# Performance work log

Measured on AMD Instinct MI355X. Metric: run time of the kernel, lower is better.

## Reference

```python
import jax, jax.numpy as jnp
import numpy as np

NUM_GRAPHS = 64

def setup_inputs() -> dict:
    key = jax.random.key(0)
    ks = jax.random.split(key, 10)
    N, E, D, V = 100000, 1600000, 64, 30
    node_types = jax.random.randint(ks[0], (N,), 0, V, dtype=jnp.int64 if jax.config.jax_enable_x64 else jnp.int32)
    edge_index = jax.random.randint(ks[1], (2, E), 0, N, dtype=jnp.int32)
    batch = jnp.sort(jax.random.randint(ks[2], (N,), 0, NUM_GRAPHS, dtype=jnp.int32))
    emb_table = jax.random.normal(ks[3], (V, D), dtype=jnp.float32)
    W1 = jax.random.normal(ks[4], (D, D), dtype=jnp.float32) / np.sqrt(D)
    W2 = jax.random.normal(ks[5], (D, D), dtype=jnp.float32) / np.sqrt(D)
    W3 = jax.random.normal(ks[6], (D, D), dtype=jnp.float32) / np.sqrt(D)
    b1 = jnp.zeros((D,), jnp.float32)
    b2 = jnp.zeros((D,), jnp.float32)
    b3 = jnp.zeros((D,), jnp.float32)
    return {"node_types": node_types, "edge_index": edge_index, "batch": batch,
            "emb_table": emb_table, "W1": W1, "b1": b1, "W2": W2, "b2": b2, "W3": W3, "b3": b3}

def _gcn_conv(x, W, b, row, col, norm, N):
    # x' = D^-1/2 (A+I) D^-1/2 (x @ W) + b   (PyG GCNConv semantics)
    h = x @ W
    msg = h[row] * norm[:, None]              # gather + edgewise scale
    out = jax.ops.segment_sum(msg, col, num_segments=N)  # scatter-add at targets
    return out + b

def reference(node_types, edge_index, batch, emb_table, W1, b1, W2, b2, W3, b3):
    N = node_types.shape[0]
    # add self-loops
    loops = jnp.arange(N, dtype=edge_index.dtype)
    row = jnp.concatenate([edge_index[0], loops])
    col = jnp.concatenate([edge_index[1], loops])
    # symmetric normalization on A + I
    deg = jax.ops.segment_sum(jnp.ones_like(col, dtype=jnp.float32), col, num_segments=N)
    dinv = jnp.where(deg > 0, jax.lax.rsqrt(deg), 0.0)
    norm = dinv[row] * dinv[col]
    x = emb_table[node_types]
    x = jax.nn.relu(_gcn_conv(x, W1, b1, row, col, norm, N))
    x = jax.nn.relu(_gcn_conv(x, W2, b2, row, col, norm, N))
    x = _gcn_conv(x, W3, b3, row, col, norm, N)
    # global mean pool over batch segments
    sums = jax.ops.segment_sum(x, batch, num_segments=NUM_GRAPHS)
    cnts = jax.ops.segment_sum(jnp.ones((N,), jnp.float32), batch, num_segments=NUM_GRAPHS)
    pooled = sums / jnp.maximum(cnts, 1.0)[:, None]
    # L2 normalize rows
    return pooled / jnp.linalg.norm(pooled, axis=1, keepdims=True)
```

## Files before the change

kernel.cpp:

```cpp
#include <hip/hip_runtime.h>
#include <hip/hip_fp16.h>

#define DD 64
#define NUM_GRAPHS 64
#define AGG_BLOCKS 2048
#define EB 512
#define BINW 256
#define MAXNB 512
#define EBIN_CAP 6144

__global__ __launch_bounds__(256) void k_hist(const int* __restrict__ col,
                                              int* __restrict__ H, int E, int NB, int CE) {
    __shared__ int h[MAXNB];
    int eb = blockIdx.x, t = threadIdx.x;
    for (int i = t; i < NB; i += 256) h[i] = 0;
    __syncthreads();
    int e0 = eb * CE, e1 = min(E, e0 + CE);
    for (int e = e0 + t; e < e1; e += 256) atomicAdd(&h[col[e] >> 8], 1);
    __syncthreads();
    for (int i = t; i < NB; i += 256) H[eb * NB + i] = h[i];
}

__global__ __launch_bounds__(256) void k_scanA(int* __restrict__ H,
                                               int* __restrict__ bintot, int NB) {
    __shared__ int s[256];
    int b = blockIdx.x, t = threadIdx.x;
    int i0 = (2 * t) * NB + b, i1 = (2 * t + 1) * NB + b;
    int v0 = H[i0], v1 = H[i1];
    int tot = v0 + v1;
    s[t] = tot;
    __syncthreads();
    for (int off = 1; off < 256; off <<= 1) {
        int tv = (t >= off) ? s[t - off] : 0;
        __syncthreads();
        s[t] += tv;
        __syncthreads();
    }
    int excl = s[t] - tot;
    H[i0] = excl;
    H[i1] = excl + v0;
    if (t == 255) bintot[b] = s[255];
}

__global__ void k_scanB(const int* __restrict__ bintot, int* __restrict__ binstart, int NB) {
    __shared__ int s[512];
    int t = threadIdx.x;
    int v = (t < NB) ? bintot[t] : 0;
    s[t] = v;
    __syncthreads();
    for (int off = 1; off < 512; off <<= 1) {
        int tv = (t >= off) ? s[t - off] : 0;
        __syncthreads();
        s[t] += tv;
        __syncthreads();
    }
    if (t < NB) binstart[t] = s[t] - v;
    if (t == 511) binstart[NB] = s[511];
}

__global__ __launch_bounds__(256) void k_scatbin(const int* __restrict__ row,
                                                 const int* __restrict__ col,
                                                 const int* __restrict__ H,
                                                 const int* __restrict__ binstart,
                                                 unsigned* __restrict__ binned,
                                                 int E, int NB, int CE) {
    __shared__ int off[MAXNB];
    int eb = blockIdx.x, t = threadIdx.x;
    for (int i = t; i < NB; i += 256) off[i] = binstart[i] + H[eb * NB + i];
    __syncthreads();
    int e0 = eb * CE, e1 = min(E, e0 + CE);
    for (int e = e0 + t; e < e1; e += 256) {
        int c = col[e], r = row[e];
        int slot = atomicAdd(&off[c >> 8], 1);
        binned[slot] = ((unsigned)(c & 255) << 24) | (unsigned)r;
    }
}

__global__ __launch_bounds__(256) void k_bincsr(const unsigned* __restrict__ binned,
                                                const int* __restrict__ binstart,
                                                const int* __restrict__ nt,
                                                int* __restrict__ srcidx,
                                                int* __restrict__ rowptr,
                                                float* __restrict__ dinv,
                                                int2* __restrict__ pk, int N, int NB) {
    __shared__ unsigned arr[EBIN_CAP];
    __shared__ int sorted_[EBIN_CAP];
    __shared__ int cnt[BINW];
    __shared__ int base[BINW];
    __shared__ int cursor[BINW];
    int b = blockIdx.x, t = threadIdx.x;
    int s0 = binstart[b], s1 = binstart[b + 1];
    int binsz = s1 - s0;
    if (binsz > EBIN_CAP) binsz = EBIN_CAP;
    cnt[t] = 0;
    for (int i = t; i < binsz; i += 256) arr[i] = binned[s0 + i];
    __syncthreads();
    for (int i = t; i < binsz; i += 256) atomicAdd(&cnt[arr[i] >> 24], 1);
    __syncthreads();
    int v = cnt[t];
    base[t] = v;
    __syncthreads();
    for (int off = 1; off < 256; off <<= 1) {
        int tv = (t >= off) ? base[t - off] : 0;
        __syncthreads();
        base[t] += tv;
        __syncthreads();
    }
    int excl = base[t] - v;
    __syncthreads();
    base[t] = excl;
    cursor[t] = excl;
    __syncthreads();
    for (int i = t; i < binsz; i += 256) {
        unsigned val = arr[i];
        int pos = atomicAdd(&cursor[val >> 24], 1);
        sorted_[pos] = (int)(val & 0xFFFFFF);
    }
    __syncthreads();
    for (int i = t; i < binsz; i += 256) srcidx[s0 + i] = sorted_[i];
    int node = b * BINW + t;
    if (node < N) {
        rowptr[node] = s0 + base[t];
        float di = rsqrtf((float)cnt[t] + 1.0f);
        dinv[node] = di;
        pk[node] = make_int2(nt[node], __float_as_int(di));
    }
    if (b == NB - 1 && t == 0) rowptr[N] = s1;
}

__global__ void k_buildepk(const int* __restrict__ srcidx, const int2* __restrict__ pk,
                           unsigned* __restrict__ epku, int E) {
    int i = blockIdx.x * blockDim.x + threadIdx.x;
    if (i >= E) return;
    int2 p = pk[srcidx[i]];
    epku[i] = ((unsigned)p.x << 16) |
              (unsigned)__half_as_ushort(__float2half(__int_as_float(p.y)));
}

__global__ void k_embW1(const float* __restrict__ emb, const float* __restrict__ W1,
                        float* __restrict__ embW1, int V) {
    __shared__ float er[DD];
    int v = blockIdx.x, j = threadIdx.x;
    er[j] = emb[v * DD + j];
    __syncthreads();
    float acc = 0.0f;
    #pragma unroll
    for (int d = 0; d < DD; ++d) acc += er[d] * W1[d * DD + j];
    embW1[v * DD + j] = acc;
}

__device__ __forceinline__ float rowmatmul(float v, const float* Wcol) {
    int vb = __float_as_int(v);
    float o0 = 0.f, o1 = 0.f, o2 = 0.f, o3 = 0.f;
    #pragma unroll
    for (int d = 0; d < DD; d += 4) {
        o0 = fmaf(__int_as_float(__builtin_amdgcn_readlane(vb, d + 0)), Wcol[d + 0], o0);
        o1 = fmaf(__int_as_float(__builtin_amdgcn_readlane(vb, d + 1)), Wcol[d + 1], o1);
        o2 = fmaf(__int_as_float(__builtin_amdgcn_readlane(vb, d + 2)), Wcol[d + 2], o2);
        o3 = fmaf(__int_as_float(__builtin_amdgcn_readlane(vb, d + 3)), Wcol[d + 3], o3);
    }
    return (o0 + o1) + (o2 + o3);
}

__device__ __forceinline__ float rowmatmul_q(float4 v, const float* Wcol) {
    float va[4] = {v.x, v.y, v.z, v.w};
    int vb[4] = {__float_as_int(v.x), __float_as_int(v.y),
                 __float_as_int(v.z), __float_as_int(v.w)};
    (void)va;
    float o0 = 0.f, o1 = 0.f, o2 = 0.f, o3 = 0.f;
    #pragma unroll
    for (int d = 0; d < DD; d += 4) {
        o0 = fmaf(__int_as_float(__builtin_amdgcn_readlane(vb[0], d >> 2)), Wcol[d + 0], o0);
        o1 = fmaf(__int_as_float(__builtin_amdgcn_readlane(vb[1], d >> 2)), Wcol[d + 1], o1);
        o2 = fmaf(__int_as_float(__builtin_amdgcn_readlane(vb[2], d >> 2)), Wcol[d + 2], o2);
        o3 = fmaf(__int_as_float(__builtin_amdgcn_readlane(vb[3], d >> 2)), Wcol[d + 3], o3);
    }
    return (o0 + o1) + (o2 + o3);
}

__device__ __forceinline__ void acc_h4(float4& a, uint2 r) {
    float2 f0 = __half22float2(*(const __half2*)&r.x);
    float2 f1 = __half22float2(*(const __half2*)&r.y);
    a.x += f0.x; a.y += f0.y; a.z += f1.x; a.w += f1.y;
}

__device__ __forceinline__ float4 gather_sum_q(const int* __restrict__ srcidx,
                                               const __half* __restrict__ Hs,
                                               int s, int e, int g, int l) {
    float4 A = {0,0,0,0}, B = {0,0,0,0}, C = {0,0,0,0}, D = {0,0,0,0};
    int k = s;
    for (; k + 16 <= e; k += 16) {
        int i0 = srcidx[k + g];
        int i1 = srcidx[k + 4 + g];
        int i2 = srcidx[k + 8 + g];
        int i3 = srcidx[k + 12 + g];
        uint2 r0 = *(const uint2*)(Hs + (long)i0 * DD + 4 * l);
        uint2 r1 = *(const uint2*)(Hs + (long)i1 * DD + 4 * l);
        uint2 r2 = *(const uint2*)(Hs + (long)i2 * DD + 4 * l);
        uint2 r3 = *(const uint2*)(Hs + (long)i3 * DD + 4 * l);
        acc_h4(A, r0); acc_h4(B, r1); acc_h4(C, r2); acc_h4(D, r3);
    }
    for (; k < e; k += 4) {
        if (k + g < e) {
            int i0 = srcidx[k + g];
            uint2 r0 = *(const uint2*)(Hs + (long)i0 * DD + 4 * l);
            acc_h4(A, r0);
        }
    }
    A.x += B.x + C.x + D.x; A.y += B.y + C.y + D.y;
    A.z += B.z + C.z + D.z; A.w += B.w + C.w + D.w;
    A.x += __shfl_xor(A.x, 16, 64); A.x += __shfl_xor(A.x, 32, 64);
    A.y += __shfl_xor(A.y, 16, 64); A.y += __shfl_xor(A.y, 32, 64);
    A.z += __shfl_xor(A.z, 16, 64); A.z += __shfl_xor(A.z, 32, 64);
    A.w += __shfl_xor(A.w, 16, 64); A.w += __shfl_xor(A.w, 32, 64);
    return A;
}

__global__ __launch_bounds__(256) void k_agg1_fused(const int* __restrict__ rowptr,
                                                    const unsigned* __restrict__ epku,
                                                    const int2* __restrict__ pk,
                                                    const float* __restrict__ embW1,
                                                    const float* __restrict__ b1,
                                                    const float* __restrict__ W2,
                                                    __half* __restrict__ OUT, int N, int V) {
    __shared__ float ew[30 * DD];
    int tid = threadIdx.x;
    for (int k = tid; k < V * DD; k += 256) ew[k] = embW1[k];
    __syncthreads();
    int j = tid & 63;
    float Wcol[DD];
    #pragma unroll
    for (int d = 0; d < DD; ++d) Wcol[d] = W2[d * DD + j];
    float bj = b1[j];
    int wave0 = blockIdx.x * 4 + (tid >> 6);
    int wstride = gridDim.x * 4;
    for (int node = __builtin_amdgcn_readfirstlane(wave0); node < N;
         node += wstride) {
        int s = rowptr[node], e = rowptr[node + 1];
        float acc = 0.0f;
        int k = s;
        for (; k + 7 < e; k += 8) {
            unsigned u0 = epku[k],   u1 = epku[k+1], u2 = epku[k+2], u3 = epku[k+3];
            unsigned u4 = epku[k+4], u5 = epku[k+5], u6 = epku[k+6], u7 = epku[k+7];
            acc += ew[(u0 >> 16) * DD + j] * __half2float(__ushort_as_half((unsigned short)(u0 & 0xFFFF)))
                 + ew[(u1 >> 16) * DD + j] * __half2float(__ushort_as_half((unsigned short)(u1 & 0xFFFF)))
                 + ew[(u2 >> 16) * DD + j] * __half2float(__ushort_as_half((unsigned short)(u2 & 0xFFFF)))
                 + ew[(u3 >> 16) * DD + j] * __half2float(__ushort_as_half((unsigned short)(u3 & 0xFFFF)));
            acc += ew[(u4 >> 16) * DD + j] * __half2float(__ushort_as_half((unsigned short)(u4 & 0xFFFF)))
                 + ew[(u5 >> 16) * DD + j] * __half2float(__ushort_as_half((unsigned short)(u5 & 0xFFFF)))
                 + ew[(u6 >> 16) * DD + j] * __half2float(__ushort_as_half((unsigned short)(u6 & 0xFFFF)))
                 + ew[(u7 >> 16) * DD + j] * __half2float(__ushort_as_half((unsigned short)(u7 & 0xFFFF)));
        }
        for (; k < e; ++k) {
            unsigned u0 = epku[k];
            acc += ew[(u0 >> 16) * DD + j] * __half2float(__ushort_as_half((unsigned short)(u0 & 0xFFFF)));
        }
        int2 pc = pk[node];
        float dc = __int_as_float(pc.y);
        float v = (acc + ew[pc.x * DD + j] * dc) * dc + bj;
        v = fmaxf(v, 0.0f);
        OUT[(long)node * DD + j] = __float2half(rowmatmul(v, Wcol) * dc);
    }
}

__global__ __launch_bounds__(256) void k_agg2_fused(const int* __restrict__ rowptr,
                                                    const int* __restrict__ srcidx,
                                                    const float* __restrict__ dinv,
                                                    const __half* __restrict__ Hs,
                                                    const float* __restrict__ b2,
                                                    const float* __restrict__ W3,
                                                    __half* __restrict__ OUT, int N) {
    int tid = threadIdx.x;
    int lane = tid & 63;
    int g = lane >> 4, l = lane & 15;
    float Wcol[DD];
    #pragma unroll
    for (int d = 0; d < DD; ++d) Wcol[d] = W3[d * DD + lane];
    float4 bq = *(const float4*)(b2 + 4 * l);
    int wave0 = blockIdx.x * 4 + (tid >> 6);
    int wstride = gridDim.x * 4;
    for (int node = __builtin_amdgcn_readfirstlane(wave0); node < N;
         node += wstride) {
        int s = rowptr[node], e = rowptr[node + 1];
        float4 acc = gather_sum_q(srcidx, Hs, s, e, g, l);
        float dc = dinv[node];
        uint2 sr = *(const uint2*)(Hs + (long)node * DD + 4 * l);
        float2 s0 = __half22float2(*(const __half2*)&sr.x);
        float2 s1 = __half22float2(*(const __half2*)&sr.y);
        float4 v;
        v.x = fmaxf((acc.x + s0.x) * dc + bq.x, 0.f);
        v.y = fmaxf((acc.y + s0.y) * dc + bq.y, 0.f);
        v.z = fmaxf((acc.z + s1.x) * dc + bq.z, 0.f);
        v.w = fmaxf((acc.w + s1.y) * dc + bq.w, 0.f);
        float o = rowmatmul_q(v, Wcol);
        OUT[(long)node * DD + lane] = __float2half(o * dc);
    }
}

__global__ __launch_bounds__(256) void k_agg3_pool(const int* __restrict__ rowptr,
                                                   const int* __restrict__ srcidx,
                                                   const float* __restrict__ dinv,
                                                   const __half* __restrict__ Hs,
                                                   const float* __restrict__ b3,
                                                   const int* __restrict__ batch,
                                                   float* __restrict__ pool,
                                                   int N, int chunk) {
    int tid = threadIdx.x;
    int lane = tid & 63;
    int g = lane >> 4, l = lane & 15;
    int w = __builtin_amdgcn_readfirstlane(blockIdx.x * 4 + (tid >> 6));
    int start = w * chunk;
    if (start >= N) return;
    int endn = min(N, start + chunk);
    float4 bq = *(const float4*)(b3 + 4 * l);
    int gcur = batch[start];
    float4 pacc = {0.f, 0.f, 0.f, 0.f};
    for (int node = start; node < endn; ++node) {
        int s = rowptr[node], e = rowptr[node + 1];
        float4 acc = gather_sum_q(srcidx, Hs, s, e, g, l);
        float dc = dinv[node];
        uint2 sr = *(const uint2*)(Hs + (long)node * DD + 4 * l);
        float2 s0 = __half22float2(*(const __half2*)&sr.x);
        float2 s1 = __half22float2(*(const __half2*)&sr.y);
        float4 v;
        v.x = (acc.x + s0.x) * dc + bq.x;
        v.y = (acc.y + s0.y) * dc + bq.y;
        v.z = (acc.z + s1.x) * dc + bq.z;
        v.w = (acc.w + s1.y) * dc + bq.w;
        int gb = batch[node];
        if (gb != gcur) {
            if (g == 0) {
                atomicAdd(&pool[gcur * DD + 4 * l + 0], pacc.x);
                atomicAdd(&pool[gcur * DD + 4 * l + 1], pacc.y);
                atomicAdd(&pool[gcur * DD + 4 * l + 2], pacc.z);
                atomicAdd(&pool[gcur * DD + 4 * l + 3], pacc.w);
            }
            gcur = gb;
            pacc = v;
        } else {
            pacc.x += v.x; pacc.y += v.y; pacc.z += v.z; pacc.w += v.w;
        }
    }
    if (g == 0) {
        atomicAdd(&pool[gcur * DD + 4 * l + 0], pacc.x);
        atomicAdd(&pool[gcur * DD + 4 * l + 1], pacc.y);
        atomicAdd(&pool[gcur * DD + 4 * l + 2], pacc.z);
        atomicAdd(&pool[gcur * DD + 4 * l + 3], pacc.w);
    }
}

__global__ void k_final(const float* __restrict__ pool, const int* __restrict__ batch,
                        float* __restrict__ out, int N) {
    int g = blockIdx.x, j = threadIdx.x;
    int lo = 0, hi = N;
    while (lo < hi) { int m = (lo + hi) >> 1; if (batch[m] < g) lo = m + 1; else hi = m; }
    int lo2 = lo; hi = N;
    while (lo2 < hi) { int m = (lo2 + hi) >> 1; if (batch[m] < g + 1) lo2 = m + 1; else hi = m; }
    float cnt = fmaxf((float)(lo2 - lo), 1.0f);
    float v = pool[g * DD + j] / cnt;
    float sq = v * v;
    #pragma unroll
    for (int off = 32; off > 0; off >>= 1) sq += __shfl_down(sq, off, 64);
    float nrm = __shfl(sq, 0, 64);
    out[g * DD + j] = v / sqrtf(nrm);
}

extern "C" void kernel_launch(void* const* d_in, const int* in_sizes, int n_in,
                              void* d_out, int out_size, void* d_ws, size_t ws_size,
                              hipStream_t stream) {
    const int*   node_types = (const int*)d_in[0];
    const int*   edge_index = (const int*)d_in[1];
    const int*   batch      = (const int*)d_in[2];
    const float* emb        = (const float*)d_in[3];
    const float* W1 = (const float*)d_in[4];
    const float* b1 = (const float*)d_in[5];
    const float* W2 = (const float*)d_in[6];
    const float* b2 = (const float*)d_in[7];
    const float* W3 = (const float*)d_in[8];
    const float* b3 = (const float*)d_in[9];
    const int N = in_sizes[0];
    const int E = in_sizes[1] / 2;
    const int V = in_sizes[3] / DD;
    const int* row = edge_index;
    const int* col = edge_index + E;
    const long ND = (long)N * DD;
    const int NB = (N + BINW - 1) / BINW;
    const int CE = (E + EB - 1) / EB;

    char* p = (char*)d_ws;
    __half*   hsA     = (__half*)p;       p += ND * sizeof(__half);
    __half*   hsB     = (__half*)p;       p += ND * sizeof(__half);
    int*      srcidx  = (int*)p;          p += (size_t)E * sizeof(int);
    unsigned* epku    = (unsigned*)p;     p += (size_t)E * sizeof(unsigned);
    unsigned* binned  = (unsigned*)p;     p += (size_t)E * sizeof(unsigned);
    int*      H       = (int*)p;          p += (size_t)EB * NB * sizeof(int);
    int*      bintot  = (int*)p;          p += (size_t)(NB + 4) * sizeof(int);
    int*      binstart= (int*)p;          p += (size_t)(NB + 4) * sizeof(int);
    float*    dinv    = (float*)p;        p += (size_t)N * sizeof(float);
    int2*     pk      = (int2*)p;         p += (size_t)N * sizeof(int2);
    int*      rowptr  = (int*)p;          p += (size_t)(N + 4) * sizeof(int);
    float*    pool    = (float*)p;        p += (size_t)NUM_GRAPHS * DD * sizeof(float);
    float*    embW1   = (float*)p;        p += (size_t)V * DD * sizeof(float);

    k_hist<<<EB, 256, 0, stream>>>(col, H, E, NB, CE);
    k_scanA<<<NB, 256, 0, stream>>>(H, bintot, NB);
    k_scanB<<<1, 512, 0, stream>>>(bintot, binstart, NB);
    k_scatbin<<<EB, 256, 0, stream>>>(row, col, H, binstart, binned, E, NB, CE);
    k_bincsr<<<NB, 256, 0, stream>>>(binned, binstart, node_types, srcidx, rowptr,
                                     dinv, pk, N, NB);
    k_buildepk<<<(E + 255) / 256, 256, 0, stream>>>(srcidx, pk, epku, E);

    k_embW1<<<V, DD, 0, stream>>>(emb, W1, embW1, V);
    k_agg1_fused<<<AGG_BLOCKS, 256, 0, stream>>>(rowptr, epku, pk, embW1, b1, W2,
                                                 hsA, N, V);
    k_agg2_fused<<<AGG_BLOCKS, 256, 0, stream>>>(rowptr, srcidx, dinv, hsA, b2, W3,
                                                 hsB, N);
    hipMemsetAsync(pool, 0, (size_t)(NUM_GRAPHS * DD) * sizeof(float), stream);
    const int totalWaves = AGG_BLOCKS * 4;
    const int chunk = (N + totalWaves - 1) / totalWaves;
    k_agg3_pool<<<AGG_BLOCKS, 256, 0, stream>>>(rowptr, srcidx, dinv, hsB, b3, batch,
                                                pool, N, chunk);
    k_final<<<NUM_GRAPHS, DD, 0, stream>>>(pool, batch, (float*)d_out, N);
}
```

Baseline: 318.0 us.

## Use packed fp16 dot2 for fused epilogue matmuls and prefetch gather rows

The W2 and W3 weight columns are pre-packed into half2 pairs by a small new kernel. The per-node 64x64 epilogue matmuls in the layer-1 and layer-2 aggregation kernels now use v_dot2 fp16 instructions with fp32 accumulate, which halves the readlane and FMA count and the per-lane weight registers. Separately, the fp16 neighbor gather loop is software-pipelined so the next 16 rows load before the current ones are accumulated. In exchange, activations and weights in the epilogue are rounded to fp16, which lowers accuracy, and the prefetch raises register pressure.

```diff
diff --git a/kernel.cpp b/kernel.cpp
--- a/kernel.cpp
+++ b/kernel.cpp
@@ -8,6 +8,13 @@
 #define BINW 256
 #define MAXNB 512
 #define EBIN_CAP 6144
+
+typedef _Float16 h2_t __attribute__((ext_vector_type(2)));
+
+__device__ __forceinline__ float fdot2u(unsigned a, unsigned b, float c) {
+    return __builtin_amdgcn_fdot2(__builtin_bit_cast(h2_t, a),
+                                  __builtin_bit_cast(h2_t, b), c, false);
+}
 
 __global__ __launch_bounds__(256) void k_hist(const int* __restrict__ col,
                                               int* __restrict__ H, int E, int NB, int CE) {
@@ -149,31 +156,41 @@
     embW1[v * DD + j] = acc;
 }
 
-__device__ __forceinline__ float rowmatmul(float v, const float* Wcol) {
-    int vb = __float_as_int(v);
+__global__ void k_packW(const float* __restrict__ W, unsigned* __restrict__ Wpk) {
+    int t = blockIdx.x * blockDim.x + threadIdx.x;
+    if (t >= 32 * DD) return;
+    int p = t >> 6, j = t & 63;
+    __half2 h = __floats2half2_rn(W[(2 * p) * DD + j], W[(2 * p + 1) * DD + j]);
+    Wpk[t] = __builtin_bit_cast(unsigned, h);
+}
+
+__device__ __forceinline__ float epi_dot_full(float v, const unsigned* Wc) {
+    float vn = __shfl_xor(v, 1, 64);
+    __half2 pr = __floats2half2_rn(v, vn);
+    int vpk = __builtin_bit_cast(int, pr);
     float o0 = 0.f, o1 = 0.f, o2 = 0.f, o3 = 0.f;
     #pragma unroll
-    for (int d = 0; d < DD; d += 4) {
-        o0 = fmaf(__int_as_float(__builtin_amdgcn_readlane(vb, d + 0)), Wcol[d + 0], o0);
-        o1 = fmaf(__int_as_float(__builtin_amdgcn_readlane(vb, d + 1)), Wcol[d + 1], o1);
-        o2 = fmaf(__int_as_float(__builtin_amdgcn_readlane(vb, d + 2)), Wcol[d + 2], o2);
-        o3 = fmaf(__int_as_float(__builtin_amdgcn_readlane(vb, d + 3)), Wcol[d + 3], o3);
+    for (int p = 0; p < 32; p += 4) {
+        o0 = fdot2u((unsigned)__builtin_amdgcn_readlane(vpk, 2 * (p + 0)), Wc[p + 0], o0);
+        o1 = fdot2u((unsigned)__builtin_amdgcn_readlane(vpk, 2 * (p + 1)), Wc[p + 1], o1);
+        o2 = fdot2u((unsigned)__builtin_amdgcn_readlane(vpk, 2 * (p + 2)), Wc[p + 2], o2);
+        o3 = fdot2u((unsigned)__builtin_amdgcn_readlane(vpk, 2 * (p + 3)), Wc[p + 3], o3);
     }
     return (o0 + o1) + (o2 + o3);
 }
 
-__device__ __forceinline__ float rowmatmul_q(float4 v, const float* Wcol) {
-    float va[4] = {v.x, v.y, v.z, v.w};
-    int vb[4] = {__float_as_int(v.x), __float_as_int(v.y),
-                 __float_as_int(v.z), __float_as_int(v.w)};
-    (void)va;
+__device__ __forceinline__ float epi_dot_q(float4 v, const unsigned* Wc) {
+    __half2 h0 = __floats2half2_rn(v.x, v.y);
+    __half2 h1 = __floats2half2_rn(v.z, v.w);
+    int vp0 = __builtin_bit_cast(int, h0);
+    int vp1 = __builtin_bit_cast(int, h1);
     float o0 = 0.f, o1 = 0.f, o2 = 0.f, o3 = 0.f;
     #pragma unroll
-    for (int d = 0; d < DD; d += 4) {
-        o0 = fmaf(__int_as_float(__builtin_amdgcn_readlane(vb[0], d >> 2)), Wcol[d + 0], o0);
-        o1 = fmaf(__int_as_float(__builtin_amdgcn_readlane(vb[1], d >> 2)), Wcol[d + 1], o1);
-        o2 = fmaf(__int_as_float(__builtin_amdgcn_readlane(vb[2], d >> 2)), Wcol[d + 2], o2);
-        o3 = fmaf(__int_as_float(__builtin_amdgcn_readlane(vb[3], d >> 2)), Wcol[d + 3], o3);
+    for (int p = 0; p < 32; p += 4) {
+        o0 = fdot2u((unsigned)__builtin_amdgcn_readlane(vp0, (p + 0) >> 1), Wc[p + 0], o0);
+        o1 = fdot2u((unsigned)__builtin_amdgcn_readlane(vp1, (p + 1) >> 1), Wc[p + 1], o1);
+        o2 = fdot2u((unsigned)__builtin_amdgcn_readlane(vp0, (p + 2) >> 1), Wc[p + 2], o2);
+        o3 = fdot2u((unsigned)__builtin_amdgcn_readlane(vp1, (p + 3) >> 1), Wc[p + 3], o3);
     }
     return (o0 + o1) + (o2 + o3);
 }
@@ -189,22 +206,27 @@
                                                int s, int e, int g, int l) {
     float4 A = {0,0,0,0}, B = {0,0,0,0}, C = {0,0,0,0}, D = {0,0,0,0};
     int k = s;
-    for (; k + 16 <= e; k += 16) {
-        int i0 = srcidx[k + g];
-        int i1 = srcidx[k + 4 + g];
-        int i2 = srcidx[k + 8 + g];
-        int i3 = srcidx[k + 12 + g];
-        uint2 r0 = *(const uint2*)(Hs + (long)i0 * DD + 4 * l);
-        uint2 r1 = *(const uint2*)(Hs + (long)i1 * DD + 4 * l);
-        uint2 r2 = *(const uint2*)(Hs + (long)i2 * DD + 4 * l);
-        uint2 r3 = *(const uint2*)(Hs + (long)i3 * DD + 4 * l);
+    int kend = s + ((e - s) & ~15);
+    if (k < kend) {
+        uint2 r0 = *(const uint2*)(Hs + (long)srcidx[k + g] * DD + 4 * l);
+        uint2 r1 = *(const uint2*)(Hs + (long)srcidx[k + 4 + g] * DD + 4 * l);
+        uint2 r2 = *(const uint2*)(Hs + (long)srcidx[k + 8 + g] * DD + 4 * l);
+        uint2 r3 = *(const uint2*)(Hs + (long)srcidx[k + 12 + g] * DD + 4 * l);
+        k += 16;
+        for (; k < kend; k += 16) {
+            uint2 n0 = *(const uint2*)(Hs + (long)srcidx[k + g] * DD + 4 * l);
+            uint2 n1 = *(const uint2*)(Hs + (long)srcidx[k + 4 + g] * DD + 4 * l);
+            uint2 n2 = *(const uint2*)(Hs + (long)srcidx[k + 8 + g] * DD + 4 * l);
+            uint2 n3 = *(const uint2*)(Hs + (long)srcidx[k + 12 + g] * DD + 4 * l);
+            acc_h4(A, r0); acc_h4(B, r1); acc_h4(C, r2); acc_h4(D, r3);
+            r0 = n0; r1 = n1; r2 = n2; r3 = n3;
+        }
         acc_h4(A, r0); acc_h4(B, r1); acc_h4(C, r2); acc_h4(D, r3);
     }
     for (; k < e; k += 4) {
         if (k + g < e) {
-            int i0 = srcidx[k + g];
-            uint2 r0 = *(const uint2*)(Hs + (long)i0 * DD + 4 * l);
-            acc_h4(A, r0);
+            uint2 rr = *(const uint2*)(Hs + (long)srcidx[k + g] * DD + 4 * l);
+            acc_h4(A, rr);
         }
     }
     A.x += B.x + C.x + D.x; A.y += B.y + C.y + D.y;
@@ -221,16 +243,16 @@
                                                     const int2* __restrict__ pk,
                                                     const float* __restrict__ embW1,
                                                     const float* __restrict__ b1,
-                                                    const float* __restrict__ W2,
+                                                    const unsigned* __restrict__ W2pk,
                                                     __half* __restrict__ OUT, int N, int V) {
     __shared__ float ew[30 * DD];
     int tid = threadIdx.x;
     for (int k = tid; k < V * DD; k += 256) ew[k] = embW1[k];
     __syncthreads();
     int j = tid & 63;
-    float Wcol[DD];
-    #pragma unroll
-    for (int d = 0; d < DD; ++d) Wcol[d] = W2[d * DD + j];
+    unsigned Wc[32];
+    #pragma unroll
+    for (int p = 0; p < 32; ++p) Wc[p] = W2pk[p * DD + j];
     float bj = b1[j];
     int wave0 = blockIdx.x * 4 + (tid >> 6);
     int wstride = gridDim.x * 4;
@@ -259,7 +281,7 @@
         float dc = __int_as_float(pc.y);
         float v = (acc + ew[pc.x * DD + j] * dc) * dc + bj;
         v = fmaxf(v, 0.0f);
-        OUT[(long)node * DD + j] = __float2half(rowmatmul(v, Wcol) * dc);
+        OUT[(long)node * DD + j] = __float2half(epi_dot_full(v, Wc) * dc);
     }
 }
 
@@ -268,14 +290,14 @@
                                                     const float* __restrict__ dinv,
                                                     const __half* __restrict__ Hs,
                                                     const float* __restrict__ b2,
-                                                    const float* __restrict__ W3,
+                                                    const unsigned* __restrict__ W3pk,
                                                     __half* __restrict__ OUT, int N) {
     int tid = threadIdx.x;
     int lane = tid & 63;
     int g = lane >> 4, l = lane & 15;
-    float Wcol[DD];
-    #pragma unroll
-    for (int d = 0; d < DD; ++d) Wcol[d] = W3[d * DD + lane];
+    unsigned Wc[32];
+    #pragma unroll
+    for (int p = 0; p < 32; ++p) Wc[p] = W3pk[p * DD + lane];
     float4 bq = *(const float4*)(b2 + 4 * l);
     int wave0 = blockIdx.x * 4 + (tid >> 6);
     int wstride = gridDim.x * 4;
@@ -292,8 +314,7 @@
         v.y = fmaxf((acc.y + s0.y) * dc + bq.y, 0.f);
         v.z = fmaxf((acc.z + s1.x) * dc + bq.z, 0.f);
         v.w = fmaxf((acc.w + s1.y) * dc + bq.w, 0.f);
-        float o = rowmatmul_q(v, Wcol);
-        OUT[(long)node * DD + lane] = __float2half(o * dc);
+        OUT[(long)node * DD + lane] = __float2half(epi_dot_q(v, Wc) * dc);
     }
 }
 
@@ -401,6 +422,8 @@
     int*      rowptr  = (int*)p;          p += (size_t)(N + 4) * sizeof(int);
     float*    pool    = (float*)p;        p += (size_t)NUM_GRAPHS * DD * sizeof(float);
     float*    embW1   = (float*)p;        p += (size_t)V * DD * sizeof(float);
+    unsigned* W2pk    = (unsigned*)p;     p += 32 * DD * sizeof(unsigned);
+    unsigned* W3pk    = (unsigned*)p;     p += 32 * DD * sizeof(unsigned);
 
     k_hist<<<EB, 256, 0, stream>>>(col, H, E, NB, CE);
     k_scanA<<<NB, 256, 0, stream>>>(H, bintot, NB);
@@ -411,9 +434,12 @@
     k_buildepk<<<(E + 255) / 256, 256, 0, stream>>>(srcidx, pk, epku, E);
 
     k_embW1<<<V, DD, 0, stream>>>(emb, W1, embW1, V);
-    k_agg1_fused<<<AGG_BLOCKS, 256, 0, stream>>>(rowptr, epku, pk, embW1, b1, W2,
+    k_packW<<<8, 256, 0, stream>>>(W2, W2pk);
+    k_packW<<<8, 256, 0, stream>>>(W3, W3pk);
+
+    k_agg1_fused<<<AGG_BLOCKS, 256, 0, stream>>>(rowptr, epku, pk, embW1, b1, W2pk,
                                                  hsA, N, V);
-    k_agg2_fused<<<AGG_BLOCKS, 256, 0, stream>>>(rowptr, srcidx, dinv, hsA, b2, W3,
+    k_agg2_fused<<<AGG_BLOCKS, 256, 0, stream>>>(rowptr, srcidx, dinv, hsA, b2, W3pk,
                                                  hsB, N);
     hipMemsetAsync(pool, 0, (size_t)(NUM_GRAPHS * DD) * sizeof(float), stream);
     const int totalWaves = AGG_BLOCKS * 4;
```

Result: faster. 307.9 us (-3.2%).
